# Kernel optimization log

Hardware: AMD Instinct MI355X
Metric: run time of the kernel (lower is better)

Reference implementation:

```python
import jax, jax.numpy as jnp
import numpy as np

# ---- hardcoded module constants (from Cyborg.__init__) ----
B, S, V = 256, 128, 512
H = 30              # number of symbol vectors
N_STACKS = 2
R = 2               # REDUNDANCY
DEPTH = 4           # stack_depth
ZERO_OFFSET = 1e-6
NAND_BIAS = 3.0
INIT_SHARPEN = 10.0
N_VECS = 1 + N_STACKS  # input vec + one peek per stack = 3
C_BIG = (H + N_STACKS) * R   # 64 choices for push_fn / calc_out
C_SMALL = 2 * R              # 4 choices for pop_op / push_op


def _cossim(a, b, eps=1e-8):
    # torch.cosine_similarity semantics: per-vector norm clamp
    na = jnp.maximum(jnp.linalg.norm(a, axis=-1, keepdims=True), eps)
    nb = jnp.maximum(jnp.linalg.norm(b, axis=-1, keepdims=True), eps)
    return jnp.sum((a / na) * (b / nb), axis=-1)


def _nand(query, w, nw_raw):
    # Fuzzy-NAND gate bank (neurallambda NAND, clip='abs').
    # query: [B, N_VECS*V], w: [C, N_VECS*V], nw_raw: [C, N_VECS] -> [B, C]
    C = w.shape[0]
    q = query.reshape(-1, 1, N_VECS, V)
    wv = w.reshape(1, C, N_VECS, V)
    cos = jnp.abs(_cossim(q, wv))                 # [B, C, N_VECS], clip='abs'
    nw = jax.nn.sigmoid(nw_raw)[None]             # interpolate sim vs NOT(sim)
    interp = nw * cos + (1.0 - nw) * (1.0 - cos)
    return jnp.prod(interp, axis=-1)              # fuzzy AND over the 3 vecs


# ---- differentiable stack (soft pointer over DEPTH slots) ----
def _read(stack, ptr):
    return jnp.einsum('bdv,bd->bv', stack, ptr)

def _push(stack, ptr, val):
    p = jnp.roll(ptr, 1, axis=1)
    s = stack * (1.0 - p)[..., None] + val[:, None, :] * p[..., None]
    return s, p

def _pop(stack, ptr):
    s = stack * (1.0 - ptr)[..., None] + ZERO_OFFSET * ptr[..., None]
    p = jnp.roll(ptr, -1, axis=1)
    return s, p

def _pop_or_nop(stack, ptr, sharp, should_pop, should_nop):
    pr = jax.nn.softmax(jnp.stack([should_pop, should_nop], -1) * sharp, axis=-1)
    ps, pp = _pop(stack, ptr)
    s = ps * pr[:, 0, None, None] + stack * pr[:, 1, None, None]
    p = pp * pr[:, 0, None] + ptr * pr[:, 1, None]
    return s, p

def _push_or_nop(stack, ptr, sharp, should_push, should_nop, val):
    pr = jax.nn.softmax(jnp.stack([should_push, should_nop], -1) * sharp, axis=-1)
    ps, pp = _push(stack, ptr, val)
    s = ps * pr[:, 0, None, None] + stack * pr[:, 1, None, None]
    p = pp * pr[:, 0, None] + ptr * pr[:, 1, None]
    return s, p


def _forward(x, syms, stack_init_vec, sharp, pop_w, pop_nw, pushop_w, pushop_nw,
             pushfn_w, pushfn_nw, calc_w, calc_nw):
    b = x.shape[0]
    # init both stacks to zero_offset, pointer at slot 0, then hard-push init vec
    stack0 = jnp.full((N_STACKS, b, DEPTH, V), ZERO_OFFSET, x.dtype)
    ptr0 = jnp.zeros((N_STACKS, b, DEPTH), x.dtype).at[:, :, 0].set(1.0)
    init_val = jnp.broadcast_to(stack_init_vec, (b, V))
    stack0, ptr0 = jax.vmap(_push, in_axes=(0, 0, None))(stack0, ptr0, init_val)

    syms_b = jnp.broadcast_to(syms, (b, H, V))

    def step(carry, inp):
        stacks, ptrs = carry                                    # [2,B,D,V], [2,B,D]
        peeks = jax.vmap(_read)(stacks, ptrs)                   # [2,B,V]
        inps = jnp.concatenate([inp, peeks[0], peeks[1]], -1)   # [B,3V]
        out_opts = jnp.concatenate(
            [syms_b, peeks[0][:, None], peeks[1][:, None]], 1)  # [B,H+2,V]
        new_s, new_p = [], []
        for k in range(N_STACKS):
            pops = _nand(inps, pop_w[k], pop_nw[k])             # [B, 2R]
            pushes = _nand(inps, pushop_w[k], pushop_nw[k])     # [B, 2R]
            pv = _nand(inps, pushfn_w[k], pushfn_nw[k]).reshape(b, H + N_STACKS, R)
            push_val = jnp.einsum('bcv,bcr->bv', out_opts, pv)
            s, p = _pop_or_nop(stacks[k], ptrs[k], sharp[k],
                               pops[:, :R].max(1), pops[:, R:].max(1))
            s, p = _push_or_nop(s, p, sharp[k],
                                pushes[:, :R].max(1), pushes[:, R:].max(1), push_val)
            new_s.append(s)
            new_p.append(p)
        stacks = jnp.stack(new_s)
        ptrs = jnp.stack(new_p)
        peeks2 = jax.vmap(_read)(stacks, ptrs)
        inps2 = jnp.concatenate([inp, peeks2[0], peeks2[1]], -1)
        out_opts2 = jnp.concatenate(
            [syms_b, peeks2[0][:, None], peeks2[1][:, None]], 1)
        cv = _nand(inps2, calc_w, calc_nw).reshape(b, H + N_STACKS, R)
        out = jnp.einsum('bcv,bcr->bv', out_opts2, cv)
        return (stacks, ptrs), out

    _, outs = jax.lax.scan(step, (stack0, ptr0), jnp.swapaxes(x, 0, 1))
    return jnp.swapaxes(outs, 0, 1)  # [B,S,V]


def setup_inputs() -> dict:
    key = jax.random.key(0)
    ks = jax.random.split(key, 12)
    siv = jax.random.normal(ks[1], (V,), jnp.float32)
    siv = siv / jnp.linalg.norm(siv)
    return {
        'x': jax.random.normal(ks[0], (B, S, V), jnp.float32),
        'syms': jax.random.normal(ks[2], (H, V), jnp.float32),
        'stack_init_vec': siv,
        'sharp': jnp.full((N_STACKS,), INIT_SHARPEN, jnp.float32),
        'pop_w': jax.random.normal(ks[3], (N_STACKS, C_SMALL, N_VECS * V), jnp.float32),
        'pop_nw': jax.random.normal(ks[4], (N_STACKS, C_SMALL, N_VECS), jnp.float32) + NAND_BIAS,
        'pushop_w': jax.random.normal(ks[5], (N_STACKS, C_SMALL, N_VECS * V), jnp.float32),
        'pushop_nw': jax.random.normal(ks[6], (N_STACKS, C_SMALL, N_VECS), jnp.float32) + NAND_BIAS,
        'pushfn_w': jax.random.normal(ks[7], (N_STACKS, C_BIG, N_VECS * V), jnp.float32),
        'pushfn_nw': jax.random.normal(ks[8], (N_STACKS, C_BIG, N_VECS), jnp.float32) + NAND_BIAS,
        'calc_w': jax.random.normal(ks[9], (C_BIG, N_VECS * V), jnp.float32),
        'calc_nw': jax.random.normal(ks[10], (C_BIG, N_VECS), jnp.float32) + NAND_BIAS,
    }


def reference(x, syms, stack_init_vec, sharp, pop_w, pop_nw, pushop_w, pushop_nw,
              pushfn_w, pushfn_nw, calc_w, calc_nw):
    return _forward(x, syms, stack_init_vec, sharp, pop_w, pop_nw, pushop_w,
                    pushop_nw, pushfn_w, pushfn_nw, calc_w, calc_nw)
```

## Files before the change

kernel.cpp:

```cpp
#include <hip/hip_runtime.h>
#include <math.h>


#define SS 128
#define VV 512
#define NROWS 208
#define ZOFF 1e-6f

#define OFF_I0   0
#define OFF_OC   (32768*208)
#define OFF_GI   (OFF_OC + 32768*32)
#define OFF_M    (OFF_GI + 2*32*208)
#define OFF_A    (OFF_M + 1024)
#define OFF_Bc   (OFF_A + 624)
#define OFF_W0   (OFF_Bc + 624)

typedef _Float16 half8 __attribute__((ext_vector_type(8)));
typedef float f32x4 __attribute__((ext_vector_type(4)));

__device__ __forceinline__ const float* w_row(int r, const float* pw, const float* pow_,
                                              const float* pfw, const float* cw) {
    if (r < 8)   return pw   + r * 1536;
    if (r < 16)  return pow_ + (r - 8) * 1536;
    if (r < 144) return pfw  + (r - 16) * 1536;
    return cw + (r - 144) * 1536;
}
__device__ __forceinline__ const float* nw_row(int r, const float* pn, const float* pon,
                                               const float* pfn, const float* cn) {
    if (r < 8)   return pn   + r * 3;
    if (r < 16)  return pon  + (r - 8) * 3;
    if (r < 144) return pfn  + (r - 16) * 3;
    return cn + (r - 144) * 3;
}

__global__ void kB(const float* __restrict__ syms, const float* __restrict__ siv,
                   const float* __restrict__ pw, const float* __restrict__ pn,
                   const float* __restrict__ pow_, const float* __restrict__ pon,
                   const float* __restrict__ pfw, const float* __restrict__ pfn,
                   const float* __restrict__ cw, const float* __restrict__ cn,
                   float* __restrict__ ws) {
    int blk = blockIdx.x, tid = threadIdx.x;
    if (blk < 64) {
        int jj = blk >> 5, e = blk & 31;
        __shared__ float bas[512];
        for (int i = tid; i < 512; i += 256)
            bas[i] = (e == 0) ? 1.0f : ((e == 1) ? siv[i] : syms[(e - 2) * 512 + i]);
        __syncthreads();
        if (tid < NROWS) {
            int c = tid;
            const float4* w4 = (const float4*)(w_row(c, pw, pow_, pfw, cw) + (jj + 1) * 512);
            const float4* b4 = (const float4*)bas;
            float s = 0.f;
            for (int q = 0; q < 128; ++q) {
                float4 a = b4[q], b = w4[q];
                s += a.x * b.x + a.y * b.y + a.z * b.z + a.w * b.w;
            }
            ws[OFF_GI + (jj * 32 + e) * 208 + c] = s;
        }
    } else if (blk == 64) {
        __shared__ float basw[32 * 512];
        for (int i = tid; i < 32 * 512; i += 256) {
            int m = i >> 9, v = i & 511;
            basw[i] = (m == 0) ? 1.0f : ((m == 1) ? siv[v] : syms[(m - 2) * 512 + v]);
        }
        __syncthreads();
        for (int p = tid; p < 1024; p += 256) {
            int m = p >> 5, mm = p & 31;
            const float4* a4 = (const float4*)(basw + m * 512);
            const float4* b4 = (const float4*)(basw + mm * 512);
            float s = 0.f;
            for (int q = 0; q < 128; ++q) {
                float4 a = a4[q], b = b4[q];
                s += a.x * b.x + a.y * b.y + a.z * b.z + a.w * b.w;
            }
            ws[OFF_M + p] = s;
        }
    } else if (blk == 65) {
        for (int idx = tid; idx < 624; idx += 256) {
            int r = idx / 3, j = idx % 3;
            const float4* w4 = (const float4*)(w_row(r, pw, pow_, pfw, cw) + j * 512);
            float s = 0.f;
            for (int q = 0; q < 128; ++q) {
                float4 b = w4[q];
                s += b.x * b.x + b.y * b.y + b.z * b.z + b.w * b.w;
            }
            float nrm = fmaxf(sqrtf(s), 1e-8f);
            float nwv = nw_row(r, pn, pon, pfn, cn)[j];
            float sig = 1.f / (1.f + expf(-nwv));
            ws[OFF_A + idx]  = (2.f * sig - 1.f) / nrm;
            ws[OFF_Bc + idx] = 1.f - sig;
        }
    } else {
        int part = blk - 66;
        _Float16* whp = (_Float16*)(ws + OFF_W0);
        _Float16* wlp = whp + 208 * 512;
        for (int i = tid; i < 6656; i += 256) {
            int flat = part * 6656 + i;
            int c = flat >> 9, v = flat & 511;
            float wv = w_row(c, pw, pow_, pfw, cw)[v];
            _Float16 h = (_Float16)wv;
            whp[flat] = h;
            wlp[flat] = (_Float16)(wv - (float)h);
        }
    }
}

__global__ __launch_bounds__(256) void kA(const float* __restrict__ x, float* __restrict__ ws) {
    __shared__ half8 AH[2][256];
    __shared__ half8 AL[2][256];
    __shared__ float red[256];
    __shared__ float invx[64];
    const int tid = threadIdx.x;
    const int wid = tid >> 6, l = tid & 63;
    const size_t bt0 = (size_t)blockIdx.x * 64;

    const int sr = tid >> 2, ss = tid & 3;
    const float* xp = x + (bt0 + sr) * 512 + ss * 8;
    const int wpos = (sr >> 4) * 64 + (sr & 15) + (ss << 4);

    const _Float16* whp = (const _Float16*)(ws + OFF_W0);
    const _Float16* wlp = whp + 208 * 512;

    const int t0 = (wid == 0) ? 0 : (1 + 3 * wid);
    const int nt = (wid == 0) ? 4 : 3;

    f32x4 acc[4][4];
#pragma unroll
    for (int m = 0; m < 4; ++m)
#pragma unroll
        for (int tt = 0; tt < 4; ++tt)
            acc[m][tt] = (f32x4){0.f, 0.f, 0.f, 0.f};

    float sumsq = 0.f;
    auto stage = [&](int kt, int buf) {
        float v[8];
        *(float4*)v       = *(const float4*)(xp + kt * 32);
        *(float4*)(v + 4) = *(const float4*)(xp + kt * 32 + 4);
        half8 hh, hl;
#pragma unroll
        for (int j = 0; j < 8; ++j) {
            sumsq += v[j] * v[j];
            _Float16 h = (_Float16)v[j];
            hh[j] = h;
            hl[j] = (_Float16)(v[j] - (float)h);
        }
        AH[buf][wpos] = hh;
        AL[buf][wpos] = hl;
    };

    stage(0, 0);
    __syncthreads();

    for (int kt = 0; kt < 16; ++kt) {
        const int buf = kt & 1;
        if (kt < 15) stage(kt + 1, buf ^ 1);

        half8 ahm[4], alm[4];
#pragma unroll
        for (int m = 0; m < 4; ++m) {
            ahm[m] = AH[buf][m * 64 + l];
            alm[m] = AL[buf][m * 64 + l];
        }
        const int kof = kt * 32 + (l >> 4) * 8;
#pragma unroll
        for (int tt = 0; tt < 4; ++tt) {
            if (tt < nt) {
                const int c = (t0 + tt) * 16 + (l & 15);
                half8 bh = *(const half8*)(whp + c * 512 + kof);
                half8 bl = *(const half8*)(wlp + c * 512 + kof);
#pragma unroll
                for (int m = 0; m < 4; ++m) {
                    acc[m][tt] = __builtin_amdgcn_mfma_f32_16x16x32_f16(ahm[m], bh, acc[m][tt], 0, 0, 0);
                    acc[m][tt] = __builtin_amdgcn_mfma_f32_16x16x32_f16(ahm[m], bl, acc[m][tt], 0, 0, 0);
                    acc[m][tt] = __builtin_amdgcn_mfma_f32_16x16x32_f16(alm[m], bh, acc[m][tt], 0, 0, 0);
                }
            }
        }
        __syncthreads();
    }

    red[tid] = sumsq;
    __syncthreads();
    if (tid < 64) {
        float s = red[tid * 4] + red[tid * 4 + 1] + red[tid * 4 + 2] + red[tid * 4 + 3];
        invx[tid] = 1.f / fmaxf(sqrtf(s), 1e-8f);
    }
    __syncthreads();

#pragma unroll
    for (int tt = 0; tt < 4; ++tt) {
        if (tt < nt) {
            const int c = (t0 + tt) * 16 + (l & 15);
            const float A0 = ws[OFF_A + c * 3];
            const float B0 = ws[OFF_Bc + c * 3];
#pragma unroll
            for (int m = 0; m < 4; ++m) {
                const int rbase = m * 16 + (l >> 4) * 4;
#pragma unroll
                for (int j = 0; j < 4; ++j) {
                    const float ix = invx[rbase + j];
                    ws[OFF_I0 + (bt0 + rbase + j) * 208 + c] = A0 * fabsf(acc[m][tt][j]) * ix + B0;
                }
            }
        }
    }
}

__global__ __attribute__((amdgpu_flat_work_group_size(256, 256), amdgpu_waves_per_eu(1, 1)))
void kC(float* __restrict__ ws, const float* __restrict__ sharp) {
    __shared__ float pkL[64];
    __shared__ float nndL[144];
    __shared__ float nnd2L[64];
    __shared__ float iqL[2];
    const int b = blockIdx.x, tid = threadIdx.x;
    const int wid = tid >> 6, l = tid & 63;
    const int k = l >> 5, m = l & 31;
    const int isRow = (tid < 144);
    const int r2 = 144 + l;

    const float* GI = ws + OFF_GI;
    float G1[64], G2[64];
    float4 Mr[8];
    float A1r = 0.f, A2r = 0.f, B1r = 0.f, B2r = 0.f;
    float A1d = 0.f, A2d = 0.f, B1d = 0.f, B2d = 0.f;
    if (isRow) {
#pragma unroll
        for (int i = 0; i < 32; ++i) {
            G1[i]      = GI[i * 208 + tid];
            G1[32 + i] = GI[(32 + i) * 208 + tid];
        }
        A1r = ws[OFF_A + tid * 3 + 1];  A2r = ws[OFF_A + tid * 3 + 2];
        B1r = ws[OFF_Bc + tid * 3 + 1]; B2r = ws[OFF_Bc + tid * 3 + 2];
    }
    if (wid == 3) {
#pragma unroll
        for (int i = 0; i < 32; ++i) {
            G2[i]      = GI[i * 208 + r2];
            G2[32 + i] = GI[(32 + i) * 208 + r2];
        }
        A1d = ws[OFF_A + r2 * 3 + 1];  A2d = ws[OFF_A + r2 * 3 + 2];
        B1d = ws[OFF_Bc + r2 * 3 + 1]; B2d = ws[OFF_Bc + r2 * 3 + 2];
    }
    if (wid == 1) {
#pragma unroll
        for (int q = 0; q < 8; ++q) Mr[q] = *(const float4*)(ws + OFF_M + m * 32 + q * 4);
    }
    const float sh = sharp[k];

    float st[4], p[4];
#pragma unroll
    for (int d = 0; d < 4; ++d) {
        st[d] = (d == 1) ? ((m == 1) ? 1.f : 0.f) : ((m == 0) ? ZOFF : 0.f);
        p[d] = (d == 1) ? 1.f : 0.f;
    }
    float pk = st[0] * p[0] + st[1] * p[1] + st[2] * p[2] + st[3] * p[3];

    const float* i0base = ws + OFF_I0 + (size_t)b * SS * 208;
    float i0r = isRow ? i0base[tid] : 0.f;
    float i0d = (wid == 3) ? i0base[r2] : 0.f;

    if (wid == 0) pkL[l] = pk;
    __syncthreads();
    if (wid == 1) {
        const float* ph = pkL + 32 * k;
        float Mv = 0.f;
#pragma unroll
        for (int q = 0; q < 8; ++q) {
            float4 mr = Mr[q];
            float4 a = *(const float4*)(ph + 4 * q);
            Mv += mr.x * a.x + mr.y * a.y + mr.z * a.z + mr.w * a.w;
        }
        float part = pk * Mv;
        part += __shfl_xor(part, 1);  part += __shfl_xor(part, 2);
        part += __shfl_xor(part, 4);  part += __shfl_xor(part, 8);
        part += __shfl_xor(part, 16);
        if ((tid & 31) == 0) iqL[k] = 1.f / fmaxf(sqrtf(part), 1e-8f);
    }
    __syncthreads();
    float iq0 = iqL[0], iq1 = iqL[1];

    for (int t = 0; t < SS; ++t) {
        const int tn = (t < SS - 1) ? (t + 1) : t;
        float i0n = 0.f;
        if (isRow) {
            i0n = i0base[(size_t)tn * 208 + tid];
            float d1 = 0.f, d2 = 0.f;
#pragma unroll
            for (int q = 0; q < 8; ++q) {
                float4 a = *(const float4*)(pkL + 4 * q);
                float4 c = *(const float4*)(pkL + 32 + 4 * q);
                d1 += a.x * G1[4*q] + a.y * G1[4*q+1] + a.z * G1[4*q+2] + a.w * G1[4*q+3];
                d2 += c.x * G1[32+4*q] + c.y * G1[33+4*q] + c.z * G1[34+4*q] + c.w * G1[35+4*q];
            }
            nndL[tid] = i0r * (A1r * fabsf(d1) * iq0 + B1r) * (A2r * fabsf(d2) * iq1 + B2r);
        }
        __syncthreads();

        float4 gp4 = *(const float4*)(nndL + 4 * k);
        float4 gq4 = *(const float4*)(nndL + 8 + 4 * k);
        float prp0 = 1.f / (1.f + __expf((fmaxf(gp4.z, gp4.w) - fmaxf(gp4.x, gp4.y)) * sh));
        float prq0 = 1.f / (1.f + __expf((fmaxf(gq4.z, gq4.w) - fmaxf(gq4.x, gq4.y)) * sh));
        float prp1 = 1.f - prp0, prq1 = 1.f - prq0;
        float prx = 0.f, pry = 0.f;
        if (m >= 2) {
            float2 pr2 = *(const float2*)(nndL + 16 + 64 * k + 2 * m - 4);
            prx = pr2.x; pry = pr2.y;
        }
        float4 t30 = *(const float4*)(nndL + 16 + 64 * k + 60);
        float pkOther = __shfl_xor(pk, 32);
        float pk0m = k ? pkOther : pk;
        float pk1m = k ? pk : pkOther;
        float pvc = prx + pry + (t30.x + t30.y) * pk0m + (t30.z + t30.w) * pk1m;

        float zc = (m == 0) ? ZOFF : 0.f;
        float s1[4], p1[4];
#pragma unroll
        for (int d = 0; d < 4; ++d) {
            float ps = st[d] * (1.f - p[d]) + zc * p[d];
            s1[d] = ps * prp0 + st[d] * prp1;
            p1[d] = p[(d + 1) & 3] * prp0 + p[d] * prp1;
        }
#pragma unroll
        for (int d = 0; d < 4; ++d) {
            float pu = p1[(d + 3) & 3];
            float su = s1[d] * (1.f - pu) + pvc * pu;
            st[d] = su * prq0 + s1[d] * prq1;
            p[d] = pu * prq0 + p1[d] * prq1;
        }
        float pkp = st[0] * p[0] + st[1] * p[1] + st[2] * p[2] + st[3] * p[3];
        if (wid == 0) pkL[l] = pkp;
        __syncthreads();

        float dd1 = 0.f, dd2 = 0.f, i0dn = 0.f;
        if (wid == 3) {
            i0dn = i0base[(size_t)tn * 208 + r2];
#pragma unroll
            for (int q = 0; q < 8; ++q) {
                float4 a = *(const float4*)(pkL + 4 * q);
                float4 c = *(const float4*)(pkL + 32 + 4 * q);
                dd1 += a.x * G2[4*q] + a.y * G2[4*q+1] + a.z * G2[4*q+2] + a.w * G2[4*q+3];
                dd2 += c.x * G2[32+4*q] + c.y * G2[33+4*q] + c.z * G2[34+4*q] + c.w * G2[35+4*q];
            }
        } else if (wid == 1) {
            const float* ph = pkL + 32 * k;
            float Mv = 0.f;
#pragma unroll
            for (int q = 0; q < 8; ++q) {
                float4 mr = Mr[q];
                float4 a = *(const float4*)(ph + 4 * q);
                Mv += mr.x * a.x + mr.y * a.y + mr.z * a.z + mr.w * a.w;
            }
            float part = pkp * Mv;
            part += __shfl_xor(part, 1);  part += __shfl_xor(part, 2);
            part += __shfl_xor(part, 4);  part += __shfl_xor(part, 8);
            part += __shfl_xor(part, 16);
            if ((tid & 31) == 0) iqL[k] = 1.f / fmaxf(sqrtf(part), 1e-8f);
        }
        __syncthreads();

        iq0 = iqL[0]; iq1 = iqL[1];
        if (wid == 3) {
            nnd2L[l] = i0d * (A1d * fabsf(dd1) * iq0 + B1d) * (A2d * fabsf(dd2) * iq1 + B2d);
            i0d = i0dn;
        }
        __syncthreads();

        float pkpOther = __shfl_xor(pkp, 32);
        if (tid < 32) {
            float cx = 0.f, cy = 0.f;
            if (m >= 2) {
                float2 c2 = *(const float2*)(nnd2L + 2 * m - 4);
                cx = c2.x; cy = c2.y;
            }
            float4 c30 = *(const float4*)(nnd2L + 60);
            float oc = cx + cy + (c30.x + c30.y) * pkp + (c30.z + c30.w) * pkpOther;
            ws[OFF_OC + ((size_t)b * SS + t) * 32 + m] = oc;
        }
        pk = pkp;
        i0r = i0n;
    }
}

__global__ __launch_bounds__(256) void kD(const float* __restrict__ ws, const float* __restrict__ syms,
                                          const float* __restrict__ siv, float* __restrict__ out) {
    int t = threadIdx.x;
    int rg = t >> 6;
    int vc = (t & 63) * 8;
    size_t r0 = (size_t)blockIdx.x * 16 + rg * 4;
    const float* oc = ws + OFF_OC;
    float acc[4][8];
    float4 sv0 = *(const float4*)(siv + vc);
    float4 sv1 = *(const float4*)(siv + vc + 4);
#pragma unroll
    for (int rr = 0; rr < 4; ++rr) {
        float c0 = oc[(r0 + rr) * 32 + 0];
        float c1 = oc[(r0 + rr) * 32 + 1];
        acc[rr][0] = c0 + c1 * sv0.x; acc[rr][1] = c0 + c1 * sv0.y;
        acc[rr][2] = c0 + c1 * sv0.z; acc[rr][3] = c0 + c1 * sv0.w;
        acc[rr][4] = c0 + c1 * sv1.x; acc[rr][5] = c0 + c1 * sv1.y;
        acc[rr][6] = c0 + c1 * sv1.z; acc[rr][7] = c0 + c1 * sv1.w;
    }
    for (int mm = 0; mm < 30; ++mm) {
        float4 b0 = *(const float4*)(syms + mm * 512 + vc);
        float4 b1 = *(const float4*)(syms + mm * 512 + vc + 4);
#pragma unroll
        for (int rr = 0; rr < 4; ++rr) {
            float c = oc[(r0 + rr) * 32 + 2 + mm];
            acc[rr][0] += c * b0.x; acc[rr][1] += c * b0.y;
            acc[rr][2] += c * b0.z; acc[rr][3] += c * b0.w;
            acc[rr][4] += c * b1.x; acc[rr][5] += c * b1.y;
            acc[rr][6] += c * b1.z; acc[rr][7] += c * b1.w;
        }
    }
#pragma unroll
    for (int rr = 0; rr < 4; ++rr) {
        float* o = out + (r0 + rr) * 512 + vc;
        *(float4*)o       = make_float4(acc[rr][0], acc[rr][1], acc[rr][2], acc[rr][3]);
        *(float4*)(o + 4) = make_float4(acc[rr][4], acc[rr][5], acc[rr][6], acc[rr][7]);
    }
}

extern "C" void kernel_launch(void* const* d_in, const int* in_sizes, int n_in,
                              void* d_out, int out_size, void* d_ws, size_t ws_size,
                              hipStream_t stream) {
    const float* x    = (const float*)d_in[0];
    const float* syms = (const float*)d_in[1];
    const float* siv  = (const float*)d_in[2];
    const float* shp  = (const float*)d_in[3];
    const float* pw   = (const float*)d_in[4];
    const float* pn   = (const float*)d_in[5];
    const float* pow_ = (const float*)d_in[6];
    const float* pon  = (const float*)d_in[7];
    const float* pfw  = (const float*)d_in[8];
    const float* pfn  = (const float*)d_in[9];
    const float* cw   = (const float*)d_in[10];
    const float* cn   = (const float*)d_in[11];
    float* ws  = (float*)d_ws;
    float* out = (float*)d_out;

    hipLaunchKernelGGL(kB, dim3(82),   dim3(256), 0, stream,
                       syms, siv, pw, pn, pow_, pon, pfw, pfn, cw, cn, ws);
    hipLaunchKernelGGL(kA, dim3(512),  dim3(256), 0, stream, x, ws);
    hipLaunchKernelGGL(kC, dim3(256),  dim3(256), 0, stream, ws, shp);
    hipLaunchKernelGGL(kD, dim3(2048), dim3(256), 0, stream, ws, syms, siv, out);
}
```

Measured before the change: 442.6 us.

## Cut per-step barriers in recurrent kernel by computing norms redundantly in every wave

```diff
diff --git a/kernel.cpp b/kernel.cpp
--- a/kernel.cpp
+++ b/kernel.cpp
@@ -210,8 +210,6 @@
 void kC(float* __restrict__ ws, const float* __restrict__ sharp) {
     __shared__ float pkL[64];
     __shared__ float nndL[144];
-    __shared__ float nnd2L[64];
-    __shared__ float iqL[2];
     const int b = blockIdx.x, tid = threadIdx.x;
     const int wid = tid >> 6, l = tid & 63;
     const int k = l >> 5, m = l & 31;
@@ -241,10 +239,9 @@
         A1d = ws[OFF_A + r2 * 3 + 1];  A2d = ws[OFF_A + r2 * 3 + 2];
         B1d = ws[OFF_Bc + r2 * 3 + 1]; B2d = ws[OFF_Bc + r2 * 3 + 2];
     }
-    if (wid == 1) {
-#pragma unroll
-        for (int q = 0; q < 8; ++q) Mr[q] = *(const float4*)(ws + OFF_M + m * 32 + q * 4);
-    }
+#pragma unroll
+    for (int q = 0; q < 8; ++q) Mr[q] = *(const float4*)(ws + OFF_M + m * 32 + q * 4);
+
     const float sh = sharp[k];
 
     float st[4], p[4];
@@ -256,46 +253,67 @@
     float pk = st[0] * p[0] + st[1] * p[1] + st[2] * p[2] + st[3] * p[3];
 
     const float* i0base = ws + OFF_I0 + (size_t)b * SS * 208;
-    float i0r = isRow ? i0base[tid] : 0.f;
-    float i0d = (wid == 3) ? i0base[r2] : 0.f;
-
-    if (wid == 0) pkL[l] = pk;
-    __syncthreads();
-    if (wid == 1) {
+    float i0r  = isRow ? i0base[tid] : 0.f;
+    float i0rn = 0.f;
+    float i0d  = (wid == 3) ? i0base[r2] : 0.f;
+
+    float iq0 = 1.f, iq1 = 1.f;
+    auto gram_iq = [&](float own) {
         const float* ph = pkL + 32 * k;
-        float Mv = 0.f;
-#pragma unroll
-        for (int q = 0; q < 8; ++q) {
-            float4 mr = Mr[q];
-            float4 a = *(const float4*)(ph + 4 * q);
-            Mv += mr.x * a.x + mr.y * a.y + mr.z * a.z + mr.w * a.w;
-        }
-        float part = pk * Mv;
+        float4 a0 = *(const float4*)(ph);
+        float4 a1 = *(const float4*)(ph + 4);
+        float4 a2 = *(const float4*)(ph + 8);
+        float4 a3 = *(const float4*)(ph + 12);
+        float4 a4 = *(const float4*)(ph + 16);
+        float4 a5 = *(const float4*)(ph + 20);
+        float4 a6 = *(const float4*)(ph + 24);
+        float4 a7 = *(const float4*)(ph + 28);
+        float mva = Mr[0].x*a0.x + Mr[0].y*a0.y + Mr[0].z*a0.z + Mr[0].w*a0.w
+                  + Mr[2].x*a2.x + Mr[2].y*a2.y + Mr[2].z*a2.z + Mr[2].w*a2.w
+                  + Mr[4].x*a4.x + Mr[4].y*a4.y + Mr[4].z*a4.z + Mr[4].w*a4.w
+                  + Mr[6].x*a6.x + Mr[6].y*a6.y + Mr[6].z*a6.z + Mr[6].w*a6.w;
+        float mvb = Mr[1].x*a1.x + Mr[1].y*a1.y + Mr[1].z*a1.z + Mr[1].w*a1.w
+                  + Mr[3].x*a3.x + Mr[3].y*a3.y + Mr[3].z*a3.z + Mr[3].w*a3.w
+                  + Mr[5].x*a5.x + Mr[5].y*a5.y + Mr[5].z*a5.z + Mr[5].w*a5.w
+                  + Mr[7].x*a7.x + Mr[7].y*a7.y + Mr[7].z*a7.z + Mr[7].w*a7.w;
+        float part = own * (mva + mvb);
         part += __shfl_xor(part, 1);  part += __shfl_xor(part, 2);
         part += __shfl_xor(part, 4);  part += __shfl_xor(part, 8);
         part += __shfl_xor(part, 16);
-        if ((tid & 31) == 0) iqL[k] = 1.f / fmaxf(sqrtf(part), 1e-8f);
-    }
+        float iqOwn = 1.f / fmaxf(sqrtf(part), 1e-8f);
+        float iqOth = __shfl_xor(iqOwn, 32);
+        iq0 = k ? iqOth : iqOwn;
+        iq1 = k ? iqOwn : iqOth;
+    };
+    auto dots = [&](const float* Gt, float& d1, float& d2) {
+        float d1a = 0.f, d1b = 0.f, d2a = 0.f, d2b = 0.f;
+#pragma unroll
+        for (int q = 0; q < 8; q += 2) {
+            float4 a = *(const float4*)(pkL + 4 * q);
+            float4 bq = *(const float4*)(pkL + 4 * q + 4);
+            float4 c = *(const float4*)(pkL + 32 + 4 * q);
+            float4 e = *(const float4*)(pkL + 32 + 4 * q + 4);
+            d1a += a.x * Gt[4*q]   + a.y * Gt[4*q+1]   + a.z * Gt[4*q+2]   + a.w * Gt[4*q+3];
+            d1b += bq.x * Gt[4*q+4] + bq.y * Gt[4*q+5] + bq.z * Gt[4*q+6] + bq.w * Gt[4*q+7];
+            d2a += c.x * Gt[32+4*q] + c.y * Gt[33+4*q] + c.z * Gt[34+4*q] + c.w * Gt[35+4*q];
+            d2b += e.x * Gt[36+4*q] + e.y * Gt[37+4*q] + e.z * Gt[38+4*q] + e.w * Gt[39+4*q];
+        }
+        d1 = d1a + d1b;
+        d2 = d2a + d2b;
+    };
+
+    if (wid == 0) pkL[l] = pk;
     __syncthreads();
-    float iq0 = iqL[0], iq1 = iqL[1];
+    gram_iq(pk);
+    if (isRow) {
+        float d1, d2;
+        dots(G1, d1, d2);
+        nndL[tid] = i0r * (A1r * fabsf(d1) * iq0 + B1r) * (A2r * fabsf(d2) * iq1 + B2r);
+        i0rn = i0base[208 + tid];
+    }
+    __syncthreads();
 
     for (int t = 0; t < SS; ++t) {
-        const int tn = (t < SS - 1) ? (t + 1) : t;
-        float i0n = 0.f;
-        if (isRow) {
-            i0n = i0base[(size_t)tn * 208 + tid];
-            float d1 = 0.f, d2 = 0.f;
-#pragma unroll
-            for (int q = 0; q < 8; ++q) {
-                float4 a = *(const float4*)(pkL + 4 * q);
-                float4 c = *(const float4*)(pkL + 32 + 4 * q);
-                d1 += a.x * G1[4*q] + a.y * G1[4*q+1] + a.z * G1[4*q+2] + a.w * G1[4*q+3];
-                d2 += c.x * G1[32+4*q] + c.y * G1[33+4*q] + c.z * G1[34+4*q] + c.w * G1[35+4*q];
-            }
-            nndL[tid] = i0r * (A1r * fabsf(d1) * iq0 + B1r) * (A2r * fabsf(d2) * iq1 + B2r);
-        }
-        __syncthreads();
-
         float4 gp4 = *(const float4*)(nndL + 4 * k);
         float4 gq4 = *(const float4*)(nndL + 8 + 4 * k);
         float prp0 = 1.f / (1.f + __expf((fmaxf(gp4.z, gp4.w) - fmaxf(gp4.x, gp4.y)) * sh));
@@ -331,53 +349,35 @@
         if (wid == 0) pkL[l] = pkp;
         __syncthreads();
 
-        float dd1 = 0.f, dd2 = 0.f, i0dn = 0.f;
+        gram_iq(pkp);
+        if (isRow) {
+            float d1, d2;
+            dots(G1, d1, d2);
+            float iv = i0rn;
+            int tn2 = (t < SS - 2) ? (t + 2) : (SS - 1);
+            i0rn = i0base[(size_t)tn2 * 208 + tid];
+            nndL[tid] = iv * (A1r * fabsf(d1) * iq0 + B1r) * (A2r * fabsf(d2) * iq1 + B2r);
+        }
         if (wid == 3) {
-            i0dn = i0base[(size_t)tn * 208 + r2];
-#pragma unroll
-            for (int q = 0; q < 8; ++q) {
-                float4 a = *(const float4*)(pkL + 4 * q);
-                float4 c = *(const float4*)(pkL + 32 + 4 * q);
-                dd1 += a.x * G2[4*q] + a.y * G2[4*q+1] + a.z * G2[4*q+2] + a.w * G2[4*q+3];
-                dd2 += c.x * G2[32+4*q] + c.y * G2[33+4*q] + c.z * G2[34+4*q] + c.w * G2[35+4*q];
-            }
-        } else if (wid == 1) {
-            const float* ph = pkL + 32 * k;
-            float Mv = 0.f;
-#pragma unroll
-            for (int q = 0; q < 8; ++q) {
-                float4 mr = Mr[q];
-                float4 a = *(const float4*)(ph + 4 * q);
-                Mv += mr.x * a.x + mr.y * a.y + mr.z * a.z + mr.w * a.w;
-            }
-            float part = pkp * Mv;
-            part += __shfl_xor(part, 1);  part += __shfl_xor(part, 2);
-            part += __shfl_xor(part, 4);  part += __shfl_xor(part, 8);
-            part += __shfl_xor(part, 16);
-            if ((tid & 31) == 0) iqL[k] = 1.f / fmaxf(sqrtf(part), 1e-8f);
+            float dd1, dd2;
+            dots(G2, dd1, dd2);
+            float nnd2 = i0d * (A1d * fabsf(dd1) * iq0 + B1d) * (A2d * fabsf(dd2) * iq1 + B2d);
+            int tn = (t < SS - 1) ? (t + 1) : (SS - 1);
+            i0d = i0base[(size_t)tn * 208 + r2];
+            int src = (m >= 2) ? (2 * m - 4) : 0;
+            float cx = __shfl(nnd2, src);
+            float cy = __shfl(nnd2, src + 1);
+            if (m < 2) { cx = 0.f; cy = 0.f; }
+            float s60 = __shfl(nnd2, 60), s61 = __shfl(nnd2, 61);
+            float s62 = __shfl(nnd2, 62), s63 = __shfl(nnd2, 63);
+            float pkpO = __shfl_xor(pkp, 32);
+            if (l < 32) {
+                float oc = cx + cy + (s60 + s61) * pkp + (s62 + s63) * pkpO;
+                ws[OFF_OC + ((size_t)b * SS + t) * 32 + m] = oc;
+            }
         }
         __syncthreads();
-
-        iq0 = iqL[0]; iq1 = iqL[1];
-        if (wid == 3) {
-            nnd2L[l] = i0d * (A1d * fabsf(dd1) * iq0 + B1d) * (A2d * fabsf(dd2) * iq1 + B2d);
-            i0d = i0dn;
-        }
-        __syncthreads();
-
-        float pkpOther = __shfl_xor(pkp, 32);
-        if (tid < 32) {
-            float cx = 0.f, cy = 0.f;
-            if (m >= 2) {
-                float2 c2 = *(const float2*)(nnd2L + 2 * m - 4);
-                cx = c2.x; cy = c2.y;
-            }
-            float4 c30 = *(const float4*)(nnd2L + 60);
-            float oc = cx + cy + (c30.x + c30.y) * pkp + (c30.z + c30.w) * pkpOther;
-            ws[OFF_OC + ((size_t)b * SS + t) * 32 + m] = oc;
-        }
         pk = pkp;
-        i0r = i0n;
     }
 }
 
```

Result: no change. 444.1 us (+0.3%).
